# Kernel tuning notes

Hardware: AMD Instinct MI355X
Metric: run time of the kernel (lower is better)

Reference implementation:

```python
import math
import jax, jax.numpy as jnp
import numpy as np

CNT_HEAD, D_IN, D_OUT, D_KEY, D_VALUE = 16, 1024, 1024, 64, 64
BATCH, SEQ = 4, 2048
IS_SCALED, IS_CAUSAL = True, True


def _xavier(key, shape, d1, d2):
    a = math.sqrt(6.0 / (d1 + d2))
    return jax.random.uniform(key, shape, jnp.float32, -a, a)


def setup_inputs() -> dict:
    key = jax.random.key(0)
    kx, kq, kk, kv, ko = jax.random.split(key, 5)
    x = jax.random.normal(kx, (BATCH, SEQ, D_IN), jnp.float32)
    mask = jnp.zeros((BATCH, SEQ), dtype=bool)  # padding mask, True = masked out
    W_q = _xavier(kq, (CNT_HEAD, D_IN, D_KEY), D_IN, CNT_HEAD * D_KEY)
    W_k = _xavier(kk, (CNT_HEAD, D_IN, D_KEY), D_IN, CNT_HEAD * D_KEY)
    W_v = _xavier(kv, (CNT_HEAD, D_IN, D_VALUE), D_IN, CNT_HEAD * D_VALUE)
    W_o = _xavier(ko, (CNT_HEAD, D_VALUE, D_OUT), CNT_HEAD * D_VALUE, D_OUT)
    return {"x": x, "mask": mask, "W_q": W_q, "W_k": W_k, "W_v": W_v, "W_o": W_o}


def reference(x, mask, W_q, W_k, W_v, W_o):
    seq_len = x.shape[-2]
    # per-head projections: (h, d_in, d) x (b, s, d_in) -> (b, h, s, d)
    Q = jnp.einsum('hjk,bsj->bhsk', W_q, x)
    K = jnp.einsum('hjk,bsj->bhsk', W_k, x)
    V = jnp.einsum('hjk,bsj->bhsk', W_v, x)
    # combined mask -> (b, 1, s, s), True = masked
    causal = jnp.triu(jnp.ones((seq_len, seq_len), dtype=bool), k=1)
    if IS_CAUSAL:
        m = mask[..., None, :] | causal  # (b, s, s)
    else:
        m = jnp.broadcast_to(mask[..., None, :], (mask.shape[0], seq_len, seq_len))
    m = m[..., None, :, :]  # (b, 1, s, s)
    scores = jnp.einsum('bhik,bhjk->bhij', Q, K)
    scores = jnp.where(m, -jnp.inf, scores)
    if IS_SCALED:
        scores = scores / math.sqrt(D_KEY)
    weights = jax.nn.softmax(scores, axis=-1)
    values = jnp.einsum('bhij,bhjd->bhid', weights, V)
    return jnp.einsum('hjk,bhlj->blk', W_o, values)
```

## Files before the change

### kernel.cpp

```cpp
#include <hip/hip_runtime.h>
#include <hip/hip_bf16.h>

typedef __attribute__((ext_vector_type(4))) float f32x4;
typedef __attribute__((ext_vector_type(8))) short s16x8;
typedef __attribute__((ext_vector_type(8))) unsigned short u16x8;
typedef __attribute__((ext_vector_type(4))) unsigned short u16x4;

#define BATCH 4
#define SEQ   2048
#define DIN   1024
#define NHEAD 16
#define QKW   2048
#define DOUT  1024

__device__ __forceinline__ unsigned short f2bf(float f) {
  __hip_bfloat16 h = __float2bfloat16(f);
  return __builtin_bit_cast(unsigned short, h);
}

__device__ __forceinline__ float fmax3(float a, float b, float c) {
  return fmaxf(fmaxf(a, b), c);
}

#if __has_builtin(__builtin_amdgcn_exp2f)
__device__ __forceinline__ float fast_exp2(float x) { return __builtin_amdgcn_exp2f(x); }
#else
__device__ __forceinline__ float fast_exp2(float x) { return exp2f(x); }
#endif

typedef const __attribute__((address_space(1))) unsigned int* gas_t;
typedef __attribute__((address_space(3))) unsigned int* las_t;
__device__ __forceinline__ void gload16(const void* g, void* l) {
  __builtin_amdgcn_global_load_lds((gas_t)g, (las_t)l, 16, 0, 0);
}

__global__ __launch_bounds__(256) void k_cvt_x(const float* __restrict__ x,
                                               unsigned short* __restrict__ xb, int n4) {
  int i = blockIdx.x * 256 + threadIdx.x;
  int stride = gridDim.x * 256;
  for (; i < n4; i += stride) {
    float4 v = reinterpret_cast<const float4*>(x)[i];
    ushort4 o;
    o.x = f2bf(v.x); o.y = f2bf(v.y); o.z = f2bf(v.z); o.w = f2bf(v.w);
    reinterpret_cast<ushort4*>(xb)[i] = o;
  }
}

__global__ __launch_bounds__(256) void k_cvt_wall(const float* __restrict__ Wq,
                                                  const float* __restrict__ Wk,
                                                  const float* __restrict__ Wv,
                                                  const float* __restrict__ Wo,
                                                  unsigned short* __restrict__ Wqkv,
                                                  unsigned short* __restrict__ Wot) {
  __shared__ float t[64][65];
  int zi = blockIdx.z;
  int c = threadIdx.x & 63, r0 = threadIdx.x >> 6;
  int hb = blockIdx.x, g0 = blockIdx.y * 64;
  if (zi < 3) {
    const float* W = (zi == 0) ? Wq : ((zi == 1) ? Wk : Wv);
    unsigned short* dst = Wqkv + (size_t)zi * 1024 * 1024;
#pragma unroll
    for (int r = r0; r < 64; r += 4)
      t[r][c] = W[hb * 65536 + (g0 + r) * 64 + c];
    __syncthreads();
#pragma unroll
    for (int k = r0; k < 64; k += 4)
      dst[(size_t)(hb * 64 + k) * 1024 + g0 + c] = f2bf(t[c][k]);
  } else {
#pragma unroll
    for (int d = r0; d < 64; d += 4)
      t[d][c] = Wo[hb * 65536 + d * 1024 + g0 + c];
    __syncthreads();
#pragma unroll
    for (int n = r0; n < 64; n += 4)
      Wot[(size_t)(g0 + n) * 1024 + hb * 64 + c] = f2bf(t[c][n]);
  }
}

template <typename OutT>
__global__ __launch_bounds__(256) void gemm_bt2(const unsigned short* __restrict__ A,
                                                const unsigned short* __restrict__ Bt,
                                                OutT* __restrict__ C, int M, int N, int K,
                                                int NC, unsigned short* __restrict__ VtOut) {
  __shared__ unsigned short As[2][128][64];
  __shared__ unsigned short Bs[2][128][64];
  int tid = threadIdx.x, w = tid >> 6, lane = tid & 63;
  int lr = lane & 15, lk = lane >> 4;
  int m0 = blockIdx.x * 128, n0 = blockIdx.y * 128;
  int wm = (w >> 1) * 64, wn = (w & 1) * 64;
  const f32x4 z = {0.f, 0.f, 0.f, 0.f};
  f32x4 acc[4][4];
#pragma unroll
  for (int m = 0; m < 4; ++m)
#pragma unroll
    for (int n = 0; n < 4; ++n) acc[m][n] = z;

  int srow = w * 32 + (lane >> 3);
  int gchunk = (lane & 7) ^ (lane >> 3);
  const unsigned short* pA = A + (size_t)(m0 + srow) * K + gchunk * 8;
  const unsigned short* pB = Bt + (size_t)(n0 + srow) * K + gchunk * 8;

#define GSTAGE(BUF, KO)                                                          \
  {                                                                              \
    _Pragma("unroll") for (int c = 0; c < 4; ++c) {                              \
      gload16(pA + (size_t)(c * 8) * K + (KO),                                   \
              (char*)&As[(BUF)][0][0] + w * 4096 + c * 1024);                    \
      gload16(pB + (size_t)(c * 8) * K + (KO),                                   \
              (char*)&Bs[(BUF)][0][0] + w * 4096 + c * 1024);                    \
    }                                                                            \
  }

  int sl0 = ((lk) ^ (lr & 7)) << 4;
  int sl1 = ((4 + lk) ^ (lr & 7)) << 4;

  GSTAGE(0, 0)
  asm volatile("s_waitcnt vmcnt(0)" ::: "memory");
  __builtin_amdgcn_s_barrier();
  asm volatile("" ::: "memory");

  const int T = K >> 6;
  int kt = 0;
#define KTILE(BUF)                                                               \
  {                                                                              \
    if (kt + 1 < T) GSTAGE((BUF) ^ 1, (kt + 1) * 64)                             \
    const char* ab = (const char*)&As[(BUF)][0][0];                              \
    const char* bb = (const char*)&Bs[(BUF)][0][0];                              \
    _Pragma("unroll") for (int ks = 0; ks < 2; ++ks) {                           \
      int so = ks ? sl1 : sl0;                                                   \
      s16x8 Af[4], Bf[4];                                                        \
      _Pragma("unroll") for (int m = 0; m < 4; ++m)                              \
        Af[m] = *reinterpret_cast<const s16x8*>(ab + (wm + m * 16 + lr) * 128 + so); \
      _Pragma("unroll") for (int n = 0; n < 4; ++n)                              \
        Bf[n] = *reinterpret_cast<const s16x8*>(bb + (wn + n * 16 + lr) * 128 + so); \
      _Pragma("unroll") for (int m = 0; m < 4; ++m)                              \
      _Pragma("unroll") for (int n = 0; n < 4; ++n)                              \
        acc[m][n] = __builtin_amdgcn_mfma_f32_16x16x32_bf16(Af[m], Bf[n],        \
                                                            acc[m][n], 0, 0, 0); \
    }                                                                            \
    asm volatile("s_waitcnt lgkmcnt(0)" ::: "memory");                           \
    asm volatile("s_waitcnt vmcnt(0)" ::: "memory");                             \
    __builtin_amdgcn_s_barrier();                                                \
    asm volatile("" ::: "memory");                                               \
    ++kt;                                                                        \
  }

  for (;;) {
    KTILE(0)
    if (kt == T) break;
    KTILE(1)
    if (kt == T) break;
  }
#undef KTILE
#undef GSTAGE

  if (VtOut != nullptr && n0 >= 2048) {
    int hh = (n0 + wn - 2048) >> 6;
    int rowb = m0 + wm;
    int bb2 = rowb >> 11;
    int sq = rowb & 2047;
#pragma unroll
    for (int m = 0; m < 4; ++m) {
      int sb = sq + ((m >> 1) & 1) * 32 + lk * 8 + (m & 1) * 4;
#pragma unroll
      for (int n = 0; n < 4; ++n) {
        int d = n * 16 + lr;
        u16x4 ov;
#pragma unroll
        for (int r = 0; r < 4; ++r) ov[r] = f2bf(acc[m][n][r]);
        *reinterpret_cast<u16x4*>(&VtOut[((size_t)(bb2 * NHEAD + hh) * 64 + d) * SEQ + sb]) = ov;
      }
    }
  } else {
#pragma unroll
    for (int m = 0; m < 4; ++m)
#pragma unroll
      for (int n = 0; n < 4; ++n)
#pragma unroll
        for (int r = 0; r < 4; ++r) {
          int row = m0 + wm + m * 16 + lk * 4 + r;
          int col = n0 + wn + n * 16 + lr;
          float v = acc[m][n][r];
          if constexpr (sizeof(OutT) == 4) C[(size_t)row * NC + col] = v;
          else C[(size_t)row * NC + col] = (OutT)f2bf(v);
        }
  }
}

__global__ __launch_bounds__(512) void attn_kernel(const unsigned short* __restrict__ QK,
                                                   const unsigned short* __restrict__ Vt,
                                                   unsigned short* __restrict__ Oa) {
  __shared__ unsigned short Ks[2][2][64 * 64];
  __shared__ unsigned short Vs[2][2][64 * 64];
  int tid = threadIdx.x, w = tid >> 6, lane = tid & 63;
  int lr = lane & 15, lk = lane >> 4;
  int bx = blockIdx.x;
  int bh = bx & 63;
  int qbi = 7 - (bx >> 6);
  int h = bh & 15, b = bh >> 4;
  int q0 = qbi * 256 + w * 32;
  const unsigned short* base = QK + (size_t)b * SEQ * QKW;
  const unsigned short* vtb = Vt + (size_t)(b * NHEAD + h) * 64 * SEQ;
  const float cl = 0.1803368801111204f;
  const f32x4 z = {0.f, 0.f, 0.f, 0.f};

  s16x8 qf[2][2];
#pragma unroll
  for (int mf = 0; mf < 2; ++mf)
#pragma unroll
    for (int kfi = 0; kfi < 2; ++kfi)
      qf[mf][kfi] = *reinterpret_cast<const s16x8*>(
          base + (size_t)(q0 + mf * 16 + lr) * QKW + h * 64 + kfi * 32 + lk * 8);

  f32x4 o[4][2], lacc[2];
#pragma unroll
  for (int nfd = 0; nfd < 4; ++nfd)
#pragma unroll
    for (int mf = 0; mf < 2; ++mf) o[nfd][mf] = z;
  lacc[0] = z; lacc[1] = z;
  float m_[2] = {-1e30f, -1e30f};
  s16x8 ones;
#pragma unroll
  for (int e = 0; e < 8; ++e) ones[e] = (short)0x3F80;

  const int nt = qbi * 2 + 2;

  int xr = (lr & 7) << 4;
  int off8[4][2];
#pragma unroll
  for (int nf = 0; nf < 4; ++nf)
#pragma unroll
    for (int kfi = 0; kfi < 2; ++kfi)
      off8[nf][kfi] = (nf * 16 + lr) * 128 + ((kfi * 64 + lk * 16) ^ xr);

  int srow0 = w * 8 + (lane >> 3);
  int cbs = ((lane & 7) * 16) ^ ((srow0 & 7) << 4);
  const char* pk0 = (const char*)(base + 1024 + h * 64 + (size_t)srow0 * QKW) + cbs;
  const char* pv0 = (const char*)(vtb + (size_t)srow0 * SEQ) + cbs;
  const size_t KSUB = (size_t)64 * QKW * 2;
  const size_t KADV = (size_t)128 * QKW * 2;
  const size_t VADV = 256;

#define STAGE(BS)                                                       \
  {                                                                     \
    gload16(pk0, (char*)&Ks[(BS)][0][0] + w * 1024);                    \
    gload16(pk0 + KSUB, (char*)&Ks[(BS)][1][0] + w * 1024);             \
    gload16(pv0, (char*)&Vs[(BS)][0][0] + w * 1024);                    \
    gload16(pv0 + 128, (char*)&Vs[(BS)][1][0] + w * 1024);              \
    pk0 += KADV; pv0 += VADV;                                           \
  }

#define SUBTILE(BI, S, KB)                                                                \
  if ((KB) <= q0 + 31) {                                                                  \
    s16x8 kfr[4][2];                                                                      \
    _Pragma("unroll") for (int nf = 0; nf < 4; ++nf)                                      \
    _Pragma("unroll") for (int kfi = 0; kfi < 2; ++kfi)                                   \
      kfr[nf][kfi] = *reinterpret_cast<const s16x8*>(                                     \
          (const char*)&Ks[(BI)][(S)][0] + off8[nf][kfi]);                                \
    f32x4 st[4][2];                                                                       \
    _Pragma("unroll") for (int nf = 0; nf < 4; ++nf)                                      \
    _Pragma("unroll") for (int mf = 0; mf < 2; ++mf)                                      \
      st[nf][mf] = __builtin_amdgcn_mfma_f32_16x16x32_bf16(kfr[nf][0], qf[mf][0], z, 0, 0, 0); \
    _Pragma("unroll") for (int nf = 0; nf < 4; ++nf)                                      \
    _Pragma("unroll") for (int mf = 0; mf < 2; ++mf)                                      \
      st[nf][mf] = __builtin_amdgcn_mfma_f32_16x16x32_bf16(kfr[nf][1], qf[mf][1],         \
                                                           st[nf][mf], 0, 0, 0);          \
    if ((KB) + 63 > q0) {                                                                 \
      _Pragma("unroll") for (int nf = 0; nf < 4; ++nf)                                    \
      _Pragma("unroll") for (int mf = 0; mf < 2; ++mf)                                    \
      _Pragma("unroll") for (int r = 0; r < 4; ++r)                                       \
        if ((KB) + nf * 16 + lk * 4 + r > q0 + mf * 16 + lr) st[nf][mf][r] = -1e30f;      \
    }                                                                                     \
    s16x8 pf[2][2];                                                                       \
    _Pragma("unroll") for (int mf = 0; mf < 2; ++mf) {                                    \
      float t0 = fmax3(st[0][mf][0], st[0][mf][1], st[0][mf][2]);                         \
      float t1 = fmax3(st[0][mf][3], st[1][mf][0], st[1][mf][1]);                         \
      float t2 = fmax3(st[1][mf][2], st[1][mf][3], st[2][mf][0]);                         \
      float t3 = fmax3(st[2][mf][1], st[2][mf][2], st[2][mf][3]);                         \
      float t4 = fmax3(st[3][mf][0], st[3][mf][1], st[3][mf][2]);                         \
      float pm = fmaxf(fmax3(t0, t1, t2), fmax3(t3, t4, st[3][mf][3]));                   \
      pm = fmaxf(pm, __shfl_xor(pm, 16));                                                 \
      pm = fmaxf(pm, __shfl_xor(pm, 32));                                                 \
      pm *= cl;                                                                           \
      if (!__all(pm <= m_[mf] + 8.0f)) {                                                  \
        float mnew = fmaxf(m_[mf], pm);                                                   \
        float sc = fast_exp2(m_[mf] - mnew);                                              \
        m_[mf] = mnew;                                                                    \
        _Pragma("unroll") for (int nfd = 0; nfd < 4; ++nfd)                               \
        _Pragma("unroll") for (int r = 0; r < 4; ++r) o[nfd][mf][r] *= sc;                \
        _Pragma("unroll") for (int r = 0; r < 4; ++r) lacc[mf][r] *= sc;                  \
      }                                                                                   \
      float p[4][4];                                                                      \
      _Pragma("unroll") for (int nf = 0; nf < 4; ++nf)                                    \
      _Pragma("unroll") for (int r = 0; r < 4; ++r)                                       \
        p[nf][r] = fast_exp2(fmaf(st[nf][mf][r], cl, -m_[mf]));                           \
      union { s16x8 v; unsigned short e[8]; } pu0, pu1;                                   \
      _Pragma("unroll") for (int j2 = 0; j2 < 4; ++j2) {                                  \
        pu0.e[j2] = f2bf(p[0][j2]);                                                       \
        pu0.e[4 + j2] = f2bf(p[1][j2]);                                                   \
        pu1.e[j2] = f2bf(p[2][j2]);                                                       \
        pu1.e[4 + j2] = f2bf(p[3][j2]);                                                   \
      }                                                                                   \
      pf[mf][0] = pu0.v;                                                                  \
      pf[mf][1] = pu1.v;                                                                  \
    }                                                                                     \
    _Pragma("unroll") for (int mf = 0; mf < 2; ++mf)                                      \
    _Pragma("unroll") for (int ks = 0; ks < 2; ++ks)                                      \
      lacc[mf] = __builtin_amdgcn_mfma_f32_16x16x32_bf16(ones, pf[mf][ks],                \
                                                         lacc[mf], 0, 0, 0);              \
    _Pragma("unroll") for (int nfd = 0; nfd < 4; ++nfd)                                   \
    _Pragma("unroll") for (int ks = 0; ks < 2; ++ks) {                                    \
      s16x8 vf = *reinterpret_cast<const s16x8*>(                                         \
          (const char*)&Vs[(BI)][(S)][0] + off8[nfd][ks]);                                \
      _Pragma("unroll") for (int mf = 0; mf < 2; ++mf)                                    \
        o[nfd][mf] = __builtin_amdgcn_mfma_f32_16x16x32_bf16(vf, pf[mf][ks],              \
                                                             o[nfd][mf], 0, 0, 0);        \
    }                                                                                     \
  }

#define TILE(BI)                                                                          \
  {                                                                                       \
    if (kt + 1 < nt) STAGE((BI) ^ 1)                                                      \
    int kb = kt * 128;                                                                    \
    SUBTILE(BI, 0, kb)                                                                    \
    SUBTILE(BI, 1, kb + 64)                                                               \
    asm volatile("s_waitcnt lgkmcnt(0)" ::: "memory");                                    \
    asm volatile("s_waitcnt vmcnt(0)" ::: "memory");                                      \
    __builtin_amdgcn_s_barrier();                                                         \
    asm volatile("" ::: "memory");                                                        \
    ++kt;                                                                                 \
  }

  STAGE(0)
  asm volatile("s_waitcnt vmcnt(0)" ::: "memory");
  __builtin_amdgcn_s_barrier();
  asm volatile("" ::: "memory");

  int kt = 0;
  for (;;) {
    TILE(0)
    if (kt == nt) break;
    TILE(1)
    if (kt == nt) break;
  }
#undef TILE
#undef SUBTILE
#undef STAGE

#pragma unroll
  for (int mf = 0; mf < 2; ++mf) {
    float inv = 1.0f / lacc[mf][0];
    size_t rowoff = (size_t)(b * SEQ + q0 + mf * 16 + lr) * 1024 + h * 64;
#pragma unroll
    for (int nfd = 0; nfd < 4; ++nfd) {
      u16x4 ov;
#pragma unroll
      for (int r = 0; r < 4; ++r) ov[r] = f2bf(o[nfd][mf][r] * inv);
      *reinterpret_cast<u16x4*>(Oa + rowoff + nfd * 16 + lk * 4) = ov;
    }
  }
}

extern "C" void kernel_launch(void* const* d_in, const int* in_sizes, int n_in,
                              void* d_out, int out_size, void* d_ws, size_t ws_size,
                              hipStream_t stream) {
  const float* x  = (const float*)d_in[0];
  const float* Wq = (const float*)d_in[2];
  const float* Wk = (const float*)d_in[3];
  const float* Wv = (const float*)d_in[4];
  const float* Wo = (const float*)d_in[5];
  float* out = (float*)d_out;

  char* ws = (char*)d_ws;
  unsigned short* xb   = (unsigned short*)(ws);
  unsigned short* Wqkv = (unsigned short*)(ws + 16777216);
  unsigned short* Wot  = (unsigned short*)(ws + 23068672);
  unsigned short* QK   = (unsigned short*)(ws + 25165824);
  unsigned short* Vt   = (unsigned short*)(ws + 58720256);
  unsigned short* Oa   = (unsigned short*)(ws + 75497472);

  k_cvt_x<<<2048, 256, 0, stream>>>(x, xb, (BATCH * SEQ * DIN) / 4);
  k_cvt_wall<<<dim3(16, 16, 4), 256, 0, stream>>>(Wq, Wk, Wv, Wo, Wqkv, Wot);

  gemm_bt2<unsigned short><<<dim3(64, 24), 256, 0, stream>>>(xb, Wqkv, QK, 8192, 3072, 1024,
                                                             2048, Vt);
  attn_kernel<<<dim3(512), 512, 0, stream>>>(QK, Vt, Oa);
  gemm_bt2<float><<<dim3(64, 8), 256, 0, stream>>>(Oa, Wot, out, 8192, 1024, 1024, 1024,
                                                   nullptr);
}
```

Baseline: 163.3 us.

## Add triple-buffered K=32 GEMM with async global-to-LDS loads for QKV projection

Adds a new GEMM kernel that uses three LDS stages of 128x32 tiles, filled by direct global-to-LDS loads with an XOR swizzle, keeping two stages in flight ahead of the MFMA compute. It is used for the fused QKV projection only, while the output projection keeps the old double-buffered kernel. The intent is to hide global memory latency better and cut LDS footprint per stage. The trade-off is a barrier every 32-wide K step, twice as many loop iterations, and hand-written waitcnt logic that must match the load counts exactly.

```diff
diff --git a/kernel.cpp b/kernel.cpp
--- a/kernel.cpp
+++ b/kernel.cpp
@@ -74,6 +74,110 @@
 #pragma unroll
     for (int n = r0; n < 64; n += 4)
       Wot[(size_t)(g0 + n) * 1024 + hb * 64 + c] = f2bf(t[c][n]);
+  }
+}
+
+template <typename OutT>
+__global__ __launch_bounds__(256) void gemm_bt3(const unsigned short* __restrict__ A,
+                                                const unsigned short* __restrict__ Bt,
+                                                OutT* __restrict__ C, int M, int N, int K,
+                                                int NC, unsigned short* __restrict__ VtOut) {
+  __shared__ unsigned short As[3][128 * 32];
+  __shared__ unsigned short Bs[3][128 * 32];
+  int tid = threadIdx.x, w = tid >> 6, lane = tid & 63;
+  int lr = lane & 15, lk = lane >> 4;
+  int m0 = blockIdx.x * 128, n0 = blockIdx.y * 128;
+  int wm = (w >> 1) * 64, wn = (w & 1) * 64;
+  const f32x4 z = {0.f, 0.f, 0.f, 0.f};
+  f32x4 acc[4][4];
+#pragma unroll
+  for (int m = 0; m < 4; ++m)
+#pragma unroll
+    for (int n = 0; n < 4; ++n) acc[m][n] = z;
+
+  int r0 = w * 32 + (lane >> 2);
+  int r1 = r0 + 16;
+  int scol = (((lane & 3) ^ ((lane >> 3) & 3)) * 8);
+  const unsigned short* pA0 = A + (size_t)(m0 + r0) * K + scol;
+  const unsigned short* pA1 = A + (size_t)(m0 + r1) * K + scol;
+  const unsigned short* pB0 = Bt + (size_t)(n0 + r0) * K + scol;
+  const unsigned short* pB1 = Bt + (size_t)(n0 + r1) * K + scol;
+
+#define GSTAGE(bi_, ko_)                                              \
+  {                                                                   \
+    gload16(pA0 + (ko_), (char*)As[bi_] + (w * 2 + 0) * 1024);        \
+    gload16(pB0 + (ko_), (char*)Bs[bi_] + (w * 2 + 0) * 1024);        \
+    gload16(pA1 + (ko_), (char*)As[bi_] + (w * 2 + 1) * 1024);        \
+    gload16(pB1 + (ko_), (char*)Bs[bi_] + (w * 2 + 1) * 1024);        \
+  }
+
+  GSTAGE(0, 0)
+  GSTAGE(1, 32)
+  asm volatile("s_waitcnt vmcnt(4)" ::: "memory");
+  __builtin_amdgcn_s_barrier();
+  asm volatile("" ::: "memory");
+
+  const int T = K >> 5;
+  int bi = 0;
+  int cka = lk ^ ((lr >> 1) & 3);
+  for (int t = 0; t < T; ++t) {
+    if (t + 2 < T) {
+      int bs = bi + 2; if (bs >= 3) bs -= 3;
+      GSTAGE(bs, (t + 2) * 32)
+    }
+    s16x8 af[4], bfr[4];
+#pragma unroll
+    for (int m = 0; m < 4; ++m)
+      af[m] = *reinterpret_cast<const s16x8*>(&As[bi][(wm + m * 16 + lr) * 32 + cka * 8]);
+#pragma unroll
+    for (int n = 0; n < 4; ++n)
+      bfr[n] = *reinterpret_cast<const s16x8*>(&Bs[bi][(wn + n * 16 + lr) * 32 + cka * 8]);
+#pragma unroll
+    for (int m = 0; m < 4; ++m)
+#pragma unroll
+      for (int n = 0; n < 4; ++n)
+        acc[m][n] = __builtin_amdgcn_mfma_f32_16x16x32_bf16(af[m], bfr[n], acc[m][n], 0, 0, 0);
+    asm volatile("s_waitcnt lgkmcnt(0)" ::: "memory");
+    if (t + 2 < T)
+      asm volatile("s_waitcnt vmcnt(4)" ::: "memory");
+    else
+      asm volatile("s_waitcnt vmcnt(0)" ::: "memory");
+    __builtin_amdgcn_s_barrier();
+    asm volatile("" ::: "memory");
+    if (++bi >= 3) bi = 0;
+  }
+#undef GSTAGE
+
+  if (VtOut != nullptr && n0 >= 2048) {
+    int hh = (n0 + wn - 2048) >> 6;
+    int rowb = m0 + wm;
+    int bb2 = rowb >> 11;
+    int sq = rowb & 2047;
+#pragma unroll
+    for (int m = 0; m < 4; ++m) {
+      int sb = sq + ((m >> 1) & 1) * 32 + lk * 8 + (m & 1) * 4;
+#pragma unroll
+      for (int n = 0; n < 4; ++n) {
+        int d = n * 16 + lr;
+        u16x4 ov;
+#pragma unroll
+        for (int r = 0; r < 4; ++r) ov[r] = f2bf(acc[m][n][r]);
+        *reinterpret_cast<u16x4*>(&VtOut[((size_t)(bb2 * NHEAD + hh) * 64 + d) * SEQ + sb]) = ov;
+      }
+    }
+  } else {
+#pragma unroll
+    for (int m = 0; m < 4; ++m)
+#pragma unroll
+      for (int n = 0; n < 4; ++n)
+#pragma unroll
+        for (int r = 0; r < 4; ++r) {
+          int row = m0 + wm + m * 16 + lk * 4 + r;
+          int col = n0 + wn + n * 16 + lr;
+          float v = acc[m][n][r];
+          if constexpr (sizeof(OutT) == 4) C[(size_t)row * NC + col] = v;
+          else C[(size_t)row * NC + col] = (OutT)f2bf(v);
+        }
   }
 }
 
@@ -381,7 +485,7 @@
   k_cvt_x<<<2048, 256, 0, stream>>>(x, xb, (BATCH * SEQ * DIN) / 4);
   k_cvt_wall<<<dim3(16, 16, 4), 256, 0, stream>>>(Wq, Wk, Wv, Wo, Wqkv, Wot);
 
-  gemm_bt2<unsigned short><<<dim3(64, 24), 256, 0, stream>>>(xb, Wqkv, QK, 8192, 3072, 1024,
+  gemm_bt3<unsigned short><<<dim3(64, 24), 256, 0, stream>>>(xb, Wqkv, QK, 8192, 3072, 1024,
                                                              2048, Vt);
   attn_kernel<<<dim3(512), 512, 0, stream>>>(QK, Vt, Oa);
   gemm_bt2<float><<<dim3(64, 8), 256, 0, stream>>>(Oa, Wot, out, 8192, 1024, 1024, 1024,
```

Result: no change. 163.1 us, median of 3 (-0.1%).
